# Kernel optimization log

Measured on AMD Instinct MI355X. Metric: run time of the kernel, lower is better.

The kernel has to match this reference:

```python
import jax, jax.numpy as jnp
import numpy as np

B_SZ, D, U, NBR, MH, RH = 16384, 256, 32, 8, 512, 256  # batch, latent, u_dim, branches, meas hidden, rnn hidden
NY = 8 * 2 + 4  # num_prod*2 + num_inj
LN_EPS = 1e-5


def setup_inputs() -> dict:
    key = jax.random.key(0)
    ks = jax.random.split(key, 16)
    inp = {
        "zt": jax.random.normal(ks[0], (B_SZ, D), jnp.float32),
        "dt": jax.random.uniform(ks[1], (1, 1), jnp.float32, 0.1, 1.0),
        "ut": jax.random.normal(ks[2], (B_SZ, U), jnp.float32),
        # stacked per-branch parameters
        "gates": jax.random.normal(ks[3], (NBR, D), jnp.float32) * 0.1,
        "W1": jax.random.normal(ks[4], (NBR, MH, D), jnp.float32) / np.sqrt(D),
        "b1": jnp.zeros((NBR, MH), jnp.float32),
        "ln_g": jnp.ones((NBR, MH), jnp.float32),
        "ln_b": jnp.zeros((NBR, MH), jnp.float32),
        "W2": jax.random.normal(ks[5], (NBR, RH, MH), jnp.float32) / np.sqrt(MH),
        "b2": jnp.zeros((NBR, RH), jnp.float32),
        "lam_r": jnp.zeros((NBR, RH), jnp.float32),
        "lam_i": jax.random.normal(ks[6], (NBR, RH), jnp.float32) * 0.1,
        "rnn_B": jax.random.normal(ks[7], (NBR, RH, RH + U), jnp.float32) / np.sqrt(RH + U),
        "W_out": jax.random.normal(ks[8], (NBR, D, RH), jnp.float32) / np.sqrt(RH),
        "C": jax.random.normal(ks[9], (NY, D), jnp.float32) / np.sqrt(D),
        "Dm": jax.random.normal(ks[10], (NY, U), jnp.float32) / np.sqrt(U),
    }
    return inp


def reference(zt, dt, ut, gates, W1, b1, ln_g, ln_b, W2, b2, lam_r, lam_i, rnn_B, W_out, C, Dm):
    ut_dt = ut * dt                                           # [B, U]
    # spectral gating, all branches at once: [NBR, B, D]
    zg = zt[None, :, :] * jax.nn.sigmoid(gates)[:, None, :]
    # measurement MLP: Linear -> LayerNorm -> GELU (exact) -> Linear
    x = jnp.einsum('nbd,nhd->nbh', zg, W1) + b1[:, None, :]   # [NBR, B, MH]
    mu = jnp.mean(x, axis=-1, keepdims=True)
    var = jnp.mean((x - mu) ** 2, axis=-1, keepdims=True)
    x = (x - mu) / jnp.sqrt(var + LN_EPS) * ln_g[:, None, :] + ln_b[:, None, :]
    x = jax.nn.gelu(x, approximate=False)
    g = jnp.einsum('nbh,nrh->nbr', x, W2) + b2[:, None, :]    # [NBR, B, RH]
    # concat control and apply input matrix B_n
    ut_b = jnp.broadcast_to(ut_dt[None], (gates.shape[0],) + ut_dt.shape)
    inp = jnp.concatenate([g, ut_b], axis=-1)                 # [NBR, B, RH+U]
    b_inp = jnp.einsum('nbi,nri->nbr', inp, rnn_B)            # [NBR, B, RH]
    # single diagonal complex RNN step from h0 = 0:
    #   h_real = 0*lam.r - 0*lam.i + b_inp = b_inp ; h_imag = 0  (lambda drops out)
    h_real = b_inp
    zt1 = jnp.einsum('nbr,ndr->bd', h_real, W_out)            # sum over branches
    yt1 = zt1 @ C.T + ut_dt @ Dm.T
    return zt1, yt1
```

## Files before the change

kernel.cpp:

```cpp
#include <hip/hip_runtime.h>
#include <math.h>

#define B_TOT 16384
#define DD    256
#define UU    32
#define NBR   8
#define MH    512
#define RH    256
#define KIN   288
#define NY    20

typedef unsigned short u16;
typedef __attribute__((ext_vector_type(8))) short bfx8;
typedef __attribute__((ext_vector_type(4))) short bfx4;
typedef __attribute__((ext_vector_type(4))) float fx4;

#define MFMA(a, b, c) __builtin_amdgcn_mfma_f32_16x16x32_bf16((a), (b), (c), 0, 0, 0)

__device__ __forceinline__ u16 f2bf(float f) {
  __bf16 h = (__bf16)f;
  return __builtin_bit_cast(u16, h);
}
__device__ __forceinline__ float fsigmoid(float x) {
  return __builtin_amdgcn_rcpf(1.f + __expf(-x));
}
__device__ __forceinline__ float fgelu(float v) {
  float t = v * v;
  float z = v * __builtin_fmaf(t, 0.07135481627f, 1.5957691216f);
  float p = __expf(z);
  return v - v * __builtin_amdgcn_rcpf(p + 1.f);
}
__device__ __forceinline__ void gload16(const void* g, void* l) {
  __builtin_amdgcn_global_load_lds((const __attribute__((address_space(1))) unsigned int*)(g),
                                   (__attribute__((address_space(3))) unsigned int*)(l),
                                   16, 0, 0);
}

__global__ __launch_bounds__(256)
void skolr_prep(const float* __restrict__ W1, const float* __restrict__ W2,
                const float* __restrict__ rnnB, const float* __restrict__ Wout,
                const float* __restrict__ gates, const float* __restrict__ zt,
                u16* __restrict__ w1g, u16* __restrict__ w2b, u16* __restrict__ bb,
                u16* __restrict__ wotb, u16* __restrict__ ztb)
{
  long i = (long)(blockIdx.x * 256 + threadIdx.x) * 8;
  const long E0 = 1048576;
  const long E1 = 2097152;
  const long E2 = 2686976;
  const long E3 = 3211264;
  const long E4 = 7405568;
  if (i >= E4) return;
  if (i < E0) {
    int n = (int)(i >> 17), h = (int)((i >> 8) & 511), d = (int)(i & 255);
    const float* gp = gates + n * DD + d;
    float4 g0 = *(const float4*)gp, g1 = *(const float4*)(gp + 4);
    float4 a = *(const float4*)(W1 + i), b = *(const float4*)(W1 + i + 4);
    bfx8 v;
    v[0] = f2bf(a.x * fsigmoid(g0.x)); v[1] = f2bf(a.y * fsigmoid(g0.y));
    v[2] = f2bf(a.z * fsigmoid(g0.z)); v[3] = f2bf(a.w * fsigmoid(g0.w));
    v[4] = f2bf(b.x * fsigmoid(g1.x)); v[5] = f2bf(b.y * fsigmoid(g1.y));
    v[6] = f2bf(b.z * fsigmoid(g1.z)); v[7] = f2bf(b.w * fsigmoid(g1.w));
    u16* dst = w1g + (size_t)n * 131072
             + ((((h >> 4) << 3) + (d >> 5)) << 9) + ((h & 15) << 3) + (((d >> 3) & 3) << 7);
    *(bfx8*)dst = v;
    return;
  }
  const float* src; u16* dst; long off;
  if (i < E1) {
    off = i - E0;
    int n = (int)(off >> 17), r = (int)((off >> 9) & 255), k = (int)(off & 511);
    src = W2 + off;
    dst = w2b + (size_t)n * 131072
        + ((((r >> 4) << 4) + (k >> 5)) << 9) + ((r & 15) << 3) + (((k >> 3) & 3) << 7);
  } else if (i < E2) {
    off = i - E1;
    int o = (int)off;
    int n = o / 73728, rem = o - n * 73728;
    int r = rem / KIN, k = rem - r * KIN;
    src = rnnB + off;
    dst = bb + (size_t)n * 73728
        + (((r >> 4) * 9 + (k >> 5)) << 9) + ((r & 15) << 3) + (((k >> 3) & 3) << 7);
  } else if (i < E3) {
    off = i - E2;
    int n = (int)(off >> 16), rem = (int)(off & 65535);
    int d = rem >> 8, r = rem & 255;
    src = Wout + off;
    dst = wotb + ((((d >> 4) << 6) + (n << 3) + (r >> 5)) << 9)
        + ((d & 15) << 3) + (((r >> 3) & 3) << 7);
  } else {
    off = i - E3;
    src = zt + off;
    dst = ztb + off;
  }
  float4 a = *(const float4*)src, b = *(const float4*)(src + 4);
  bfx8 v;
  v[0] = f2bf(a.x); v[1] = f2bf(a.y); v[2] = f2bf(a.z); v[3] = f2bf(a.w);
  v[4] = f2bf(b.x); v[5] = f2bf(b.y); v[6] = f2bf(b.z); v[7] = f2bf(b.w);
  *(bfx8*)dst = v;
}

__global__ __launch_bounds__(512, 2)
void skolr_fused(const u16* __restrict__ ztb, const float* __restrict__ dtp,
                 const float* __restrict__ ut,
                 const u16* __restrict__ w1g, const float* __restrict__ b1,
                 const float* __restrict__ lng, const float* __restrict__ lnb,
                 const u16* __restrict__ w2g, const float* __restrict__ b2v,
                 const u16* __restrict__ rnnb, u16* __restrict__ bing)
{
  __shared__ __align__(16) char smX[65536];
  __shared__ __align__(16) float smR[1024];
  const int tid = threadIdx.x;
  const int w  = tid >> 6;
  const int l  = tid & 63;
  const int lr = l & 15;
  const int lg = l >> 4;
  const int n  = blockIdx.x;
  const int b0 = blockIdx.y * 64;

  #pragma unroll
  for (int j = 0; j < 4; ++j) {
    int q = (w << 2) + j;
    int r = (q << 1) + (l >> 5);
    const u16* src = ztb + (size_t)(b0 + r) * DD + (((l & 31) ^ (r & 7)) << 3);
    gload16(src, smX + (q << 10));
  }
  __syncthreads();

  fx4 acc1[4][4];
  #pragma unroll
  for (int mt = 0; mt < 4; ++mt)
    #pragma unroll
    for (int nt = 0; nt < 4; ++nt)
      acc1[mt][nt] = (fx4){0.f, 0.f, 0.f, 0.f};
  {
    const u16* w1pk = w1g + (size_t)n * 131072;
    #pragma unroll
    for (int kk = 0; kk < 8; ++kk) {
      bfx8 bfr[4];
      #pragma unroll
      for (int nt = 0; nt < 4; ++nt) {
        int b = nt * 16 + lr;
        bfr[nt] = *(const bfx8*)(smX + b * 512 + ((((kk << 2) + lg) ^ (b & 7)) << 4));
      }
      #pragma unroll
      for (int mt = 0; mt < 4; ++mt) {
        int mtile = (mt < 2 ? (w << 1) + mt : 16 + (w << 1) + (mt - 2));
        bfx8 af = *(const bfx8*)(w1pk + (((mtile << 3) + kk) << 9) + (l << 3));
        #pragma unroll
        for (int nt = 0; nt < 4; ++nt)
          acc1[mt][nt] = MFMA(af, bfr[nt], acc1[mt][nt]);
      }
    }
  }
  #pragma unroll
  for (int mt = 0; mt < 4; ++mt) {
    int hb = (mt < 2 ? (w << 5) + mt * 16 : 256 + (w << 5) + (mt - 2) * 16) + (lg << 2);
    fx4 bv = *(const fx4*)(b1 + n * MH + hb);
    #pragma unroll
    for (int nt = 0; nt < 4; ++nt)
      acc1[mt][nt] += bv;
  }

  #pragma unroll
  for (int nt = 0; nt < 4; ++nt) {
    float s1 = 0.f, s2 = 0.f;
    #pragma unroll
    for (int mt = 0; mt < 4; ++mt)
      #pragma unroll
      for (int r = 0; r < 4; ++r) { float v = acc1[mt][nt][r]; s1 += v; s2 += v * v; }
    s1 += __shfl_xor(s1, 16); s1 += __shfl_xor(s1, 32);
    s2 += __shfl_xor(s2, 16); s2 += __shfl_xor(s2, 32);
    if (l < 16) { smR[w * 64 + nt * 16 + l] = s1; smR[512 + w * 64 + nt * 16 + l] = s2; }
  }
  __syncthreads();

  float meanv[4], rstdv[4];
  #pragma unroll
  for (int nt = 0; nt < 4; ++nt) {
    float ms = 0.f, ss = 0.f;
    #pragma unroll
    for (int wv = 0; wv < 8; ++wv) {
      ms += smR[wv * 64 + nt * 16 + lr];
      ss += smR[512 + wv * 64 + nt * 16 + lr];
    }
    float mean = ms * (1.f / 512.f);
    meanv[nt] = mean;
    rstdv[nt] = rsqrtf(ss * (1.f / 512.f) - mean * mean + 1e-5f);
  }
  #pragma unroll
  for (int mt = 0; mt < 4; ++mt) {
    int htile = (mt < 2 ? (w << 5) + mt * 16 : 256 + (w << 5) + (mt - 2) * 16);
    int hb = htile + (lg << 2);
    fx4 g4 = *(const fx4*)(lng + n * MH + hb);
    fx4 e4 = *(const fx4*)(lnb + n * MH + hb);
    #pragma unroll
    for (int nt = 0; nt < 4; ++nt) {
      #pragma unroll
      for (int r = 0; r < 4; ++r) {
        float v = (acc1[mt][nt][r] - meanv[nt]) * rstdv[nt] * g4[r] + e4[r];
        acc1[mt][nt][r] = fgelu(v);
      }
      int b = nt * 16 + lr;
      bfx4 p;
      p[0] = f2bf(acc1[mt][nt][0]); p[1] = f2bf(acc1[mt][nt][1]);
      p[2] = f2bf(acc1[mt][nt][2]); p[3] = f2bf(acc1[mt][nt][3]);
      int chunk6 = (htile >> 3) + (lg >> 1);
      *(bfx4*)(smX + b * 1024 + ((chunk6 ^ (b & 7)) << 4) + ((lg & 1) << 3)) = p;
    }
  }
  __syncthreads();

  const int r0 = w << 5;
  fx4 acc2[2][4];
  #pragma unroll
  for (int mt = 0; mt < 2; ++mt)
    #pragma unroll
    for (int nt = 0; nt < 4; ++nt)
      acc2[mt][nt] = (fx4){0.f, 0.f, 0.f, 0.f};
  {
    const u16* w2pk = w2g + (size_t)n * 131072;
    #pragma unroll
    for (int kk = 0; kk < 16; ++kk) {
      bfx8 xb[4];
      #pragma unroll
      for (int nt = 0; nt < 4; ++nt) {
        int b = nt * 16 + lr;
        xb[nt] = *(const bfx8*)(smX + b * 1024 + ((((kk << 2) + lg) ^ (b & 7)) << 4));
      }
      #pragma unroll
      for (int mt = 0; mt < 2; ++mt) {
        bfx8 af = *(const bfx8*)(w2pk + (((((w << 1) + mt) << 4) + kk) << 9) + (l << 3));
        #pragma unroll
        for (int nt = 0; nt < 4; ++nt)
          acc2[mt][nt] = MFMA(af, xb[nt], acc2[mt][nt]);
      }
    }
  }
  #pragma unroll
  for (int mt = 0; mt < 2; ++mt) {
    fx4 bz = *(const fx4*)(b2v + n * RH + r0 + mt * 16 + (lg << 2));
    #pragma unroll
    for (int nt = 0; nt < 4; ++nt)
      acc2[mt][nt] += bz;
  }
  __syncthreads();

  #pragma unroll
  for (int mt = 0; mt < 2; ++mt)
    #pragma unroll
    for (int nt = 0; nt < 4; ++nt) {
      int b = nt * 16 + lr;
      bfx4 p;
      p[0] = f2bf(acc2[mt][nt][0]); p[1] = f2bf(acc2[mt][nt][1]);
      p[2] = f2bf(acc2[mt][nt][2]); p[3] = f2bf(acc2[mt][nt][3]);
      int chunk5 = ((r0 + mt * 16) >> 3) + (lg >> 1);
      *(bfx4*)(smX + b * 512 + ((chunk5 ^ (b & 7)) << 4) + ((lg & 1) << 3)) = p;
    }
  __syncthreads();

  const float dtv = dtp[0];
  bfx8 ufrag[4];
  #pragma unroll
  for (int nt = 0; nt < 4; ++nt) {
    const float* up = ut + (size_t)(b0 + nt * 16 + lr) * UU + (lg << 3);
    float4 u0 = *(const float4*)up;
    float4 u1 = *(const float4*)(up + 4);
    bfx8 v;
    v[0] = f2bf(u0.x * dtv); v[1] = f2bf(u0.y * dtv);
    v[2] = f2bf(u0.z * dtv); v[3] = f2bf(u0.w * dtv);
    v[4] = f2bf(u1.x * dtv); v[5] = f2bf(u1.y * dtv);
    v[6] = f2bf(u1.z * dtv); v[7] = f2bf(u1.w * dtv);
    ufrag[nt] = v;
  }

  fx4 acc3[2][4];
  #pragma unroll
  for (int mt = 0; mt < 2; ++mt)
    #pragma unroll
    for (int nt = 0; nt < 4; ++nt)
      acc3[mt][nt] = (fx4){0.f, 0.f, 0.f, 0.f};
  {
    const u16* rpk = rnnb + (size_t)n * 73728;
    #pragma unroll
    for (int kk = 0; kk < 8; ++kk) {
      bfx8 gb[4];
      #pragma unroll
      for (int nt = 0; nt < 4; ++nt) {
        int b = nt * 16 + lr;
        gb[nt] = *(const bfx8*)(smX + b * 512 + ((((kk << 2) + lg) ^ (b & 7)) << 4));
      }
      #pragma unroll
      for (int mt = 0; mt < 2; ++mt) {
        bfx8 af = *(const bfx8*)(rpk + (((((w << 1) + mt) * 9) + kk) << 9) + (l << 3));
        #pragma unroll
        for (int nt = 0; nt < 4; ++nt)
          acc3[mt][nt] = MFMA(af, gb[nt], acc3[mt][nt]);
      }
    }
    #pragma unroll
    for (int mt = 0; mt < 2; ++mt) {
      bfx8 af = *(const bfx8*)(rpk + (((((w << 1) + mt) * 9) + 8) << 9) + (l << 3));
      #pragma unroll
      for (int nt = 0; nt < 4; ++nt)
        acc3[mt][nt] = MFMA(af, ufrag[nt], acc3[mt][nt]);
    }
  }
  #pragma unroll
  for (int mt = 0; mt < 2; ++mt)
    #pragma unroll
    for (int nt = 0; nt < 4; ++nt) {
      int b = nt * 16 + lr;
      bfx4 p;
      p[0] = f2bf(acc3[mt][nt][0]); p[1] = f2bf(acc3[mt][nt][1]);
      p[2] = f2bf(acc3[mt][nt][2]); p[3] = f2bf(acc3[mt][nt][3]);
      int chunk5 = ((r0 + mt * 16) >> 3) + (lg >> 1);
      *(bfx4*)(smX + 32768 + b * 512 + ((chunk5 ^ (b & 7)) << 4) + ((lg & 1) << 3)) = p;
    }
  __syncthreads();

  {
    int c = tid & 31;
    #pragma unroll
    for (int j = 0; j < 4; ++j) {
      int row = (tid >> 5) + j * 16;
      int4 v = *(const int4*)(smX + 32768 + row * 512 + (c << 4));
      *(int4*)(bing + (size_t)(b0 + row) * 2048 + n * 256 + c * 8) = v;
    }
  }
}

__global__ __launch_bounds__(512, 2)
void skolr_final(const u16* __restrict__ bing, const u16* __restrict__ wotb,
                 const float* __restrict__ ut, const float* __restrict__ dtp,
                 const float* __restrict__ Cm, const float* __restrict__ Dm,
                 float* __restrict__ outp)
{
  __shared__ __align__(16) char sB[65536];
  const int tid = threadIdx.x;
  const int w  = tid >> 6;
  const int l  = tid & 63;
  const int lr = l & 15;
  const int lg = l >> 4;
  const int b0 = blockIdx.x * 64;

  fx4 acc[2][4];
  #pragma unroll
  for (int mt = 0; mt < 2; ++mt)
    #pragma unroll
    for (int nt = 0; nt < 4; ++nt)
      acc[mt][nt] = (fx4){0.f, 0.f, 0.f, 0.f};

  const int srow = tid >> 5;
  const int scol = tid & 31;
  #define STAGE(buf, ks)                                                        \
    {                                                                           \
      _Pragma("unroll")                                                         \
      for (int j = 0; j < 4; ++j) {                                             \
        const u16* src = bing + (size_t)(b0 + j * 16 + srow) * 2048             \
                              + ((ks) << 8) + (scol << 3);                      \
        void* ldst = sB + (buf) * 32768 + (j << 13) + (w << 10);                \
        gload16(src, ldst);                                                     \
      }                                                                         \
    }

  STAGE(0, 0)
  for (int ks = 0; ks < 8; ++ks) {
    if (ks < 7) {
      STAGE((ks + 1) & 1, ks + 1)
      asm volatile("s_waitcnt vmcnt(4)" ::: "memory");
    } else {
      asm volatile("s_waitcnt vmcnt(0)" ::: "memory");
    }
    __builtin_amdgcn_s_barrier();
    const char* cur = sB + (ks & 1) * 32768;
    #pragma unroll
    for (int kk = 0; kk < 8; ++kk) {
      bfx8 bf[4];
      #pragma unroll
      for (int nt = 0; nt < 4; ++nt) {
        int b = nt * 16 + lr;
        bf[nt] = *(const bfx8*)(cur + b * 512 + ((((kk << 2) + lg) ^ (b & 7)) << 4));
      }
      #pragma unroll
      for (int mt = 0; mt < 2; ++mt) {
        bfx8 af = *(const bfx8*)(wotb + (((((w << 1) + mt) << 6) + (ks << 3) + kk) << 9) + (l << 3));
        #pragma unroll
        for (int nt = 0; nt < 4; ++nt)
          acc[mt][nt] = MFMA(af, bf[nt], acc[mt][nt]);
      }
    }
    __builtin_amdgcn_s_barrier();
  }

  #pragma unroll
  for (int mt = 0; mt < 2; ++mt)
    #pragma unroll
    for (int nt = 0; nt < 4; ++nt) {
      int bl = nt * 16 + lr;
      int d  = (w << 5) + mt * 16 + (lg << 2);
      *(fx4*)(outp + (size_t)(b0 + bl) * DD + d) = acc[mt][nt];
      bfx4 p;
      p[0] = f2bf(acc[mt][nt][0]); p[1] = f2bf(acc[mt][nt][1]);
      p[2] = f2bf(acc[mt][nt][2]); p[3] = f2bf(acc[mt][nt][3]);
      int chunk5 = d >> 3;
      *(bfx4*)(sB + bl * 512 + ((chunk5 ^ (bl & 7)) << 4) + ((lg & 1) << 3)) = p;
    }
  __syncthreads();

  const float dtv = dtp[0];
  for (int i = tid; i < 64 * NY; i += 512) {
    int b = i / NY;
    int y = i - b * NY;
    float s = 0.f;
    #pragma unroll 4
    for (int dc = 0; dc < 32; ++dc) {
      bfx8 zv = *(const bfx8*)(sB + b * 512 + ((dc ^ (b & 7)) << 4));
      const float* cp = Cm + y * DD + dc * 8;
      float4 c0 = *(const float4*)cp;
      float4 c1 = *(const float4*)(cp + 4);
      float z0 = (float)__builtin_bit_cast(__bf16, (u16)zv[0]);
      float z1 = (float)__builtin_bit_cast(__bf16, (u16)zv[1]);
      float z2 = (float)__builtin_bit_cast(__bf16, (u16)zv[2]);
      float z3 = (float)__builtin_bit_cast(__bf16, (u16)zv[3]);
      float z4 = (float)__builtin_bit_cast(__bf16, (u16)zv[4]);
      float z5 = (float)__builtin_bit_cast(__bf16, (u16)zv[5]);
      float z6 = (float)__builtin_bit_cast(__bf16, (u16)zv[6]);
      float z7 = (float)__builtin_bit_cast(__bf16, (u16)zv[7]);
      s += z0 * c0.x + z1 * c0.y + z2 * c0.z + z3 * c0.w;
      s += z4 * c1.x + z5 * c1.y + z6 * c1.z + z7 * c1.w;
    }
    const float* up = ut + (size_t)(b0 + b) * UU;
    const float* dp = Dm + y * UU;
    float s2 = 0.f;
    #pragma unroll
    for (int u = 0; u < UU; u += 4) {
      float4 uu = *(const float4*)(up + u);
      float4 dd = *(const float4*)(dp + u);
      s2 += uu.x * dd.x + uu.y * dd.y + uu.z * dd.z + uu.w * dd.w;
    }
    outp[(size_t)B_TOT * DD + (size_t)(b0 + b) * NY + y] = s + dtv * s2;
  }
}

extern "C" void kernel_launch(void* const* d_in, const int* in_sizes, int n_in,
                              void* d_out, int out_size, void* d_ws, size_t ws_size,
                              hipStream_t stream)
{
  (void)in_sizes; (void)n_in; (void)out_size; (void)ws_size;
  const float* zt    = (const float*)d_in[0];
  const float* dtp   = (const float*)d_in[1];
  const float* ut    = (const float*)d_in[2];
  const float* gates = (const float*)d_in[3];
  const float* W1    = (const float*)d_in[4];
  const float* b1    = (const float*)d_in[5];
  const float* lng   = (const float*)d_in[6];
  const float* lnb   = (const float*)d_in[7];
  const float* W2    = (const float*)d_in[8];
  const float* b2    = (const float*)d_in[9];
  const float* rnnB  = (const float*)d_in[12];
  const float* Wout  = (const float*)d_in[13];
  const float* Cm    = (const float*)d_in[14];
  const float* Dm    = (const float*)d_in[15];
  float* outp = (float*)d_out;
  char* ws = (char*)d_ws;

  u16* w1g  = (u16*)(ws + 0);
  u16* w2b  = (u16*)(ws + 2097152);
  u16* bb   = (u16*)(ws + 4194304);
  u16* wotb = (u16*)(ws + 5373952);
  u16* ztb  = (u16*)(ws + 6422528);
  u16* bing = (u16*)(ws + 14811136);

  skolr_prep<<<3616, 256, 0, stream>>>(W1, W2, rnnB, Wout, gates, zt,
                                       w1g, w2b, bb, wotb, ztb);
  skolr_fused<<<dim3(8, 256), 512, 0, stream>>>(ztb, dtp, ut, w1g, b1, lng, lnb,
                                                w2b, b2, bb, bing);
  skolr_final<<<256, 512, 0, stream>>>(bing, wotb, ut, dtp, Cm, Dm, outp);
}
```

Before: 316.7 us.

## Shrink fused kernel tile to 32 rows with 256 threads and split LDS staging

The fused MLP/RNN kernel now processes 32 batch rows per block with 4 waves instead of 64 rows with 8 waves. Shared memory drops from 64KB to 32KB by splitting the GELU activations into two halves: the first half is staged into one buffer, the second half into another, and the second GEMM runs in two K-phases. This is meant to raise occupancy and the number of blocks per CU. The cost is that each weight fragment is reused across fewer batch columns, so global weight traffic per output rises, and there are more barriers.

```diff
diff --git a/kernel.cpp b/kernel.cpp
--- a/kernel.cpp
+++ b/kernel.cpp
@@ -99,7 +99,7 @@
   *(bfx8*)dst = v;
 }
 
-__global__ __launch_bounds__(512, 2)
+__global__ __launch_bounds__(256, 4)
 void skolr_fused(const u16* __restrict__ ztb, const float* __restrict__ dtp,
                  const float* __restrict__ ut,
                  const u16* __restrict__ w1g, const float* __restrict__ b1,
@@ -107,161 +107,181 @@
                  const u16* __restrict__ w2g, const float* __restrict__ b2v,
                  const u16* __restrict__ rnnb, u16* __restrict__ bing)
 {
-  __shared__ __align__(16) char smX[65536];
-  __shared__ __align__(16) float smR[1024];
+  __shared__ __align__(16) char smX[32768];
+  __shared__ __align__(16) float smR[256];
   const int tid = threadIdx.x;
   const int w  = tid >> 6;
   const int l  = tid & 63;
   const int lr = l & 15;
   const int lg = l >> 4;
   const int n  = blockIdx.x;
-  const int b0 = blockIdx.y * 64;
+  const int b0 = blockIdx.y * 32;
+  char* P = smX;
+  char* Q = smX + 16384;
 
   #pragma unroll
   for (int j = 0; j < 4; ++j) {
-    int q = (w << 2) + j;
+    int q = (j << 2) + w;
     int r = (q << 1) + (l >> 5);
     const u16* src = ztb + (size_t)(b0 + r) * DD + (((l & 31) ^ (r & 7)) << 3);
-    gload16(src, smX + (q << 10));
-  }
-  __syncthreads();
-
-  fx4 acc1[4][4];
-  #pragma unroll
-  for (int mt = 0; mt < 4; ++mt)
-    #pragma unroll
-    for (int nt = 0; nt < 4; ++nt)
+    gload16(src, P + (q << 10));
+  }
+  __syncthreads();
+
+  fx4 acc1[8][2];
+  #pragma unroll
+  for (int mt = 0; mt < 8; ++mt)
+    #pragma unroll
+    for (int nt = 0; nt < 2; ++nt)
       acc1[mt][nt] = (fx4){0.f, 0.f, 0.f, 0.f};
   {
     const u16* w1pk = w1g + (size_t)n * 131072;
     #pragma unroll
     for (int kk = 0; kk < 8; ++kk) {
-      bfx8 bfr[4];
-      #pragma unroll
-      for (int nt = 0; nt < 4; ++nt) {
+      bfx8 bfr[2];
+      #pragma unroll
+      for (int nt = 0; nt < 2; ++nt) {
         int b = nt * 16 + lr;
-        bfr[nt] = *(const bfx8*)(smX + b * 512 + ((((kk << 2) + lg) ^ (b & 7)) << 4));
-      }
-      #pragma unroll
-      for (int mt = 0; mt < 4; ++mt) {
-        int mtile = (mt < 2 ? (w << 1) + mt : 16 + (w << 1) + (mt - 2));
+        bfr[nt] = *(const bfx8*)(P + b * 512 + ((((kk << 2) + lg) ^ (b & 7)) << 4));
+      }
+      #pragma unroll
+      for (int mt = 0; mt < 8; ++mt) {
+        int mtile = (mt < 4 ? (w << 2) + mt : 16 + (w << 2) + (mt - 4));
         bfx8 af = *(const bfx8*)(w1pk + (((mtile << 3) + kk) << 9) + (l << 3));
         #pragma unroll
-        for (int nt = 0; nt < 4; ++nt)
+        for (int nt = 0; nt < 2; ++nt)
           acc1[mt][nt] = MFMA(af, bfr[nt], acc1[mt][nt]);
       }
     }
   }
   #pragma unroll
-  for (int mt = 0; mt < 4; ++mt) {
-    int hb = (mt < 2 ? (w << 5) + mt * 16 : 256 + (w << 5) + (mt - 2) * 16) + (lg << 2);
+  for (int mt = 0; mt < 8; ++mt) {
+    int hb = (mt < 4 ? (w << 6) + mt * 16 : 256 + (w << 6) + (mt - 4) * 16) + (lg << 2);
     fx4 bv = *(const fx4*)(b1 + n * MH + hb);
     #pragma unroll
-    for (int nt = 0; nt < 4; ++nt)
+    for (int nt = 0; nt < 2; ++nt)
       acc1[mt][nt] += bv;
   }
 
   #pragma unroll
-  for (int nt = 0; nt < 4; ++nt) {
+  for (int nt = 0; nt < 2; ++nt) {
     float s1 = 0.f, s2 = 0.f;
     #pragma unroll
-    for (int mt = 0; mt < 4; ++mt)
+    for (int mt = 0; mt < 8; ++mt)
       #pragma unroll
       for (int r = 0; r < 4; ++r) { float v = acc1[mt][nt][r]; s1 += v; s2 += v * v; }
     s1 += __shfl_xor(s1, 16); s1 += __shfl_xor(s1, 32);
     s2 += __shfl_xor(s2, 16); s2 += __shfl_xor(s2, 32);
-    if (l < 16) { smR[w * 64 + nt * 16 + l] = s1; smR[512 + w * 64 + nt * 16 + l] = s2; }
-  }
-  __syncthreads();
-
-  float meanv[4], rstdv[4];
-  #pragma unroll
-  for (int nt = 0; nt < 4; ++nt) {
+    if (l < 16) { smR[(w << 5) + nt * 16 + l] = s1; smR[128 + (w << 5) + nt * 16 + l] = s2; }
+  }
+  __syncthreads();
+
+  float meanv[2], rstdv[2];
+  #pragma unroll
+  for (int nt = 0; nt < 2; ++nt) {
     float ms = 0.f, ss = 0.f;
     #pragma unroll
-    for (int wv = 0; wv < 8; ++wv) {
-      ms += smR[wv * 64 + nt * 16 + lr];
-      ss += smR[512 + wv * 64 + nt * 16 + lr];
+    for (int wv = 0; wv < 4; ++wv) {
+      ms += smR[(wv << 5) + nt * 16 + lr];
+      ss += smR[128 + (wv << 5) + nt * 16 + lr];
     }
     float mean = ms * (1.f / 512.f);
     meanv[nt] = mean;
     rstdv[nt] = rsqrtf(ss * (1.f / 512.f) - mean * mean + 1e-5f);
   }
   #pragma unroll
-  for (int mt = 0; mt < 4; ++mt) {
-    int htile = (mt < 2 ? (w << 5) + mt * 16 : 256 + (w << 5) + (mt - 2) * 16);
-    int hb = htile + (lg << 2);
+  for (int mt = 0; mt < 8; ++mt) {
+    int hb = (mt < 4 ? (w << 6) + mt * 16 : 256 + (w << 6) + (mt - 4) * 16) + (lg << 2);
     fx4 g4 = *(const fx4*)(lng + n * MH + hb);
     fx4 e4 = *(const fx4*)(lnb + n * MH + hb);
     #pragma unroll
-    for (int nt = 0; nt < 4; ++nt) {
+    for (int nt = 0; nt < 2; ++nt)
       #pragma unroll
       for (int r = 0; r < 4; ++r) {
         float v = (acc1[mt][nt][r] - meanv[nt]) * rstdv[nt] * g4[r] + e4[r];
         acc1[mt][nt][r] = fgelu(v);
       }
+  }
+
+  #pragma unroll
+  for (int mt = 0; mt < 4; ++mt)
+    #pragma unroll
+    for (int nt = 0; nt < 2; ++nt) {
       int b = nt * 16 + lr;
       bfx4 p;
       p[0] = f2bf(acc1[mt][nt][0]); p[1] = f2bf(acc1[mt][nt][1]);
       p[2] = f2bf(acc1[mt][nt][2]); p[3] = f2bf(acc1[mt][nt][3]);
-      int chunk6 = (htile >> 3) + (lg >> 1);
-      *(bfx4*)(smX + b * 1024 + ((chunk6 ^ (b & 7)) << 4) + ((lg & 1) << 3)) = p;
-    }
-  }
-  __syncthreads();
-
-  const int r0 = w << 5;
-  fx4 acc2[2][4];
-  #pragma unroll
-  for (int mt = 0; mt < 2; ++mt)
-    #pragma unroll
-    for (int nt = 0; nt < 4; ++nt)
+      int ch = (w << 3) + (mt << 1) + (lg >> 1);
+      *(bfx4*)(Q + b * 512 + ((ch ^ (b & 7)) << 4) + ((lg & 1) << 3)) = p;
+    }
+  __syncthreads();
+
+  fx4 acc2[4][2];
+  #pragma unroll
+  for (int mt = 0; mt < 4; ++mt)
+    #pragma unroll
+    for (int nt = 0; nt < 2; ++nt)
       acc2[mt][nt] = (fx4){0.f, 0.f, 0.f, 0.f};
-  {
-    const u16* w2pk = w2g + (size_t)n * 131072;
-    #pragma unroll
-    for (int kk = 0; kk < 16; ++kk) {
-      bfx8 xb[4];
-      #pragma unroll
-      for (int nt = 0; nt < 4; ++nt) {
-        int b = nt * 16 + lr;
-        xb[nt] = *(const bfx8*)(smX + b * 1024 + ((((kk << 2) + lg) ^ (b & 7)) << 4));
-      }
-      #pragma unroll
-      for (int mt = 0; mt < 2; ++mt) {
-        bfx8 af = *(const bfx8*)(w2pk + (((((w << 1) + mt) << 4) + kk) << 9) + (l << 3));
-        #pragma unroll
-        for (int nt = 0; nt < 4; ++nt)
-          acc2[mt][nt] = MFMA(af, xb[nt], acc2[mt][nt]);
-      }
-    }
-  }
-  #pragma unroll
-  for (int mt = 0; mt < 2; ++mt) {
-    fx4 bz = *(const fx4*)(b2v + n * RH + r0 + mt * 16 + (lg << 2));
-    #pragma unroll
-    for (int nt = 0; nt < 4; ++nt)
-      acc2[mt][nt] += bz;
-  }
-  __syncthreads();
-
-  #pragma unroll
-  for (int mt = 0; mt < 2; ++mt)
-    #pragma unroll
-    for (int nt = 0; nt < 4; ++nt) {
+  const u16* w2pk = w2g + (size_t)n * 131072;
+  #pragma unroll
+  for (int kk = 0; kk < 8; ++kk) {
+    bfx8 xb[2];
+    #pragma unroll
+    for (int nt = 0; nt < 2; ++nt) {
+      int b = nt * 16 + lr;
+      xb[nt] = *(const bfx8*)(Q + b * 512 + ((((kk << 2) + lg) ^ (b & 7)) << 4));
+    }
+    #pragma unroll
+    for (int mt = 0; mt < 4; ++mt) {
+      bfx8 af = *(const bfx8*)(w2pk + (((((w << 2) + mt) << 4) + kk) << 9) + (l << 3));
+      #pragma unroll
+      for (int nt = 0; nt < 2; ++nt)
+        acc2[mt][nt] = MFMA(af, xb[nt], acc2[mt][nt]);
+    }
+  }
+  __syncthreads();
+
+  #pragma unroll
+  for (int mt = 4; mt < 8; ++mt)
+    #pragma unroll
+    for (int nt = 0; nt < 2; ++nt) {
       int b = nt * 16 + lr;
       bfx4 p;
-      p[0] = f2bf(acc2[mt][nt][0]); p[1] = f2bf(acc2[mt][nt][1]);
-      p[2] = f2bf(acc2[mt][nt][2]); p[3] = f2bf(acc2[mt][nt][3]);
-      int chunk5 = ((r0 + mt * 16) >> 3) + (lg >> 1);
-      *(bfx4*)(smX + b * 512 + ((chunk5 ^ (b & 7)) << 4) + ((lg & 1) << 3)) = p;
-    }
-  __syncthreads();
+      p[0] = f2bf(acc1[mt][nt][0]); p[1] = f2bf(acc1[mt][nt][1]);
+      p[2] = f2bf(acc1[mt][nt][2]); p[3] = f2bf(acc1[mt][nt][3]);
+      int ch = (w << 3) + ((mt - 4) << 1) + (lg >> 1);
+      *(bfx4*)(P + b * 512 + ((ch ^ (b & 7)) << 4) + ((lg & 1) << 3)) = p;
+    }
+  __syncthreads();
+
+  #pragma unroll
+  for (int kk = 8; kk < 16; ++kk) {
+    bfx8 xb[2];
+    #pragma unroll
+    for (int nt = 0; nt < 2; ++nt) {
+      int b = nt * 16 + lr;
+      xb[nt] = *(const bfx8*)(P + b * 512 + (((((kk - 8) << 2) + lg) ^ (b & 7)) << 4));
+    }
+    #pragma unroll
+    for (int mt = 0; mt < 4; ++mt) {
+      bfx8 af = *(const bfx8*)(w2pk + (((((w << 2) + mt) << 4) + kk) << 9) + (l << 3));
+      #pragma unroll
+      for (int nt = 0; nt < 2; ++nt)
+        acc2[mt][nt] = MFMA(af, xb[nt], acc2[mt][nt]);
+    }
+  }
+  #pragma unroll
+  for (int mt = 0; mt < 4; ++mt) {
+    fx4 bz = *(const fx4*)(b2v + n * RH + (w << 6) + mt * 16 + (lg << 2));
+    #pragma unroll
+    for (int nt = 0; nt < 2; ++nt)
+      acc2[mt][nt] += bz;
+  }
 
   const float dtv = dtp[0];
-  bfx8 ufrag[4];
-  #pragma unroll
-  for (int nt = 0; nt < 4; ++nt) {
+  bfx8 ufrag[2];
+  #pragma unroll
+  for (int nt = 0; nt < 2; ++nt) {
     const float* up = ut + (size_t)(b0 + nt * 16 + lr) * UU + (lg << 3);
     float4 u0 = *(const float4*)up;
     float4 u1 = *(const float4*)(up + 4);
@@ -273,59 +293,71 @@
     ufrag[nt] = v;
   }
 
-  fx4 acc3[2][4];
-  #pragma unroll
-  for (int mt = 0; mt < 2; ++mt)
-    #pragma unroll
-    for (int nt = 0; nt < 4; ++nt)
+  #pragma unroll
+  for (int mt = 0; mt < 4; ++mt)
+    #pragma unroll
+    for (int nt = 0; nt < 2; ++nt) {
+      int b = nt * 16 + lr;
+      bfx4 p;
+      p[0] = f2bf(acc2[mt][nt][0]); p[1] = f2bf(acc2[mt][nt][1]);
+      p[2] = f2bf(acc2[mt][nt][2]); p[3] = f2bf(acc2[mt][nt][3]);
+      int ch = (w << 3) + (mt << 1) + (lg >> 1);
+      *(bfx4*)(Q + b * 512 + ((ch ^ (b & 7)) << 4) + ((lg & 1) << 3)) = p;
+    }
+  __syncthreads();
+
+  fx4 acc3[4][2];
+  #pragma unroll
+  for (int mt = 0; mt < 4; ++mt)
+    #pragma unroll
+    for (int nt = 0; nt < 2; ++nt)
       acc3[mt][nt] = (fx4){0.f, 0.f, 0.f, 0.f};
   {
     const u16* rpk = rnnb + (size_t)n * 73728;
     #pragma unroll
     for (int kk = 0; kk < 8; ++kk) {
-      bfx8 gb[4];
-      #pragma unroll
-      for (int nt = 0; nt < 4; ++nt) {
+      bfx8 gb[2];
+      #pragma unroll
+      for (int nt = 0; nt < 2; ++nt) {
         int b = nt * 16 + lr;
-        gb[nt] = *(const bfx8*)(smX + b * 512 + ((((kk << 2) + lg) ^ (b & 7)) << 4));
-      }
-      #pragma unroll
-      for (int mt = 0; mt < 2; ++mt) {
-        bfx8 af = *(const bfx8*)(rpk + (((((w << 1) + mt) * 9) + kk) << 9) + (l << 3));
+        gb[nt] = *(const bfx8*)(Q + b * 512 + ((((kk << 2) + lg) ^ (b & 7)) << 4));
+      }
+      #pragma unroll
+      for (int mt = 0; mt < 4; ++mt) {
+        bfx8 af = *(const bfx8*)(rpk + (((((w << 2) + mt) * 9) + kk) << 9) + (l << 3));
         #pragma unroll
-        for (int nt = 0; nt < 4; ++nt)
+        for (int nt = 0; nt < 2; ++nt)
           acc3[mt][nt] = MFMA(af, gb[nt], acc3[mt][nt]);
       }
     }
     #pragma unroll
-    for (int mt = 0; mt < 2; ++mt) {
-      bfx8 af = *(const bfx8*)(rpk + (((((w << 1) + mt) * 9) + 8) << 9) + (l << 3));
-      #pragma unroll
-      for (int nt = 0; nt < 4; ++nt)
+    for (int mt = 0; mt < 4; ++mt) {
+      bfx8 af = *(const bfx8*)(rpk + (((((w << 2) + mt) * 9) + 8) << 9) + (l << 3));
+      #pragma unroll
+      for (int nt = 0; nt < 2; ++nt)
         acc3[mt][nt] = MFMA(af, ufrag[nt], acc3[mt][nt]);
     }
   }
-  #pragma unroll
-  for (int mt = 0; mt < 2; ++mt)
-    #pragma unroll
-    for (int nt = 0; nt < 4; ++nt) {
+
+  #pragma unroll
+  for (int mt = 0; mt < 4; ++mt)
+    #pragma unroll
+    for (int nt = 0; nt < 2; ++nt) {
       int b = nt * 16 + lr;
       bfx4 p;
       p[0] = f2bf(acc3[mt][nt][0]); p[1] = f2bf(acc3[mt][nt][1]);
       p[2] = f2bf(acc3[mt][nt][2]); p[3] = f2bf(acc3[mt][nt][3]);
-      int chunk5 = ((r0 + mt * 16) >> 3) + (lg >> 1);
-      *(bfx4*)(smX + 32768 + b * 512 + ((chunk5 ^ (b & 7)) << 4) + ((lg & 1) << 3)) = p;
-    }
-  __syncthreads();
-
-  {
+      int ch = (w << 3) + (mt << 1) + (lg >> 1);
+      *(bfx4*)(P + b * 512 + ((ch ^ (b & 7)) << 4) + ((lg & 1) << 3)) = p;
+    }
+  __syncthreads();
+
+  #pragma unroll
+  for (int j = 0; j < 4; ++j) {
+    int row = (tid >> 5) + (j << 3);
     int c = tid & 31;
-    #pragma unroll
-    for (int j = 0; j < 4; ++j) {
-      int row = (tid >> 5) + j * 16;
-      int4 v = *(const int4*)(smX + 32768 + row * 512 + (c << 4));
-      *(int4*)(bing + (size_t)(b0 + row) * 2048 + n * 256 + c * 8) = v;
-    }
+    int4 v = *(const int4*)(P + row * 512 + (c << 4));
+    *(int4*)(bing + (size_t)(b0 + row) * 2048 + n * 256 + c * 8) = v;
   }
 }
 
@@ -473,7 +505,7 @@
 
   skolr_prep<<<3616, 256, 0, stream>>>(W1, W2, rnnB, Wout, gates, zt,
                                        w1g, w2b, bb, wotb, ztb);
-  skolr_fused<<<dim3(8, 256), 512, 0, stream>>>(ztb, dtp, ut, w1g, b1, lng, lnb,
+  skolr_fused<<<dim3(8, 512), 256, 0, stream>>>(ztb, dtp, ut, w1g, b1, lng, lnb,
                                                 w2b, b2, bb, bing);
   skolr_final<<<256, 512, 0, stream>>>(bing, wotb, ut, dtp, Cm, Dm, outp);
 }
```

Result: slower. 388.5 us (+22.7%).

## Fuse per-branch W_out GEMM into main kernel and reduce partials separately

Applied to the files above, without the earlier changes.

Moves the W_out projection into the fused per-branch kernel, so each block multiplies its own branch's RNN output by that branch's W_out slice and writes a bf16 partial zt1 per branch. A new lightweight kernel sums the eight branch partials in fp32, writes zt1, and computes yt1 from an fp32 shared-memory copy. This removes the separate 2048-wide K-loop GEMM kernel and its double-buffered staging. In exchange, the fused kernel does more work and bf16 rounding now happens per branch before summation.

```diff
diff --git a/kernel.cpp b/kernel.cpp
--- a/kernel.cpp
+++ b/kernel.cpp
@@ -20,6 +20,10 @@
 __device__ __forceinline__ u16 f2bf(float f) {
   __bf16 h = (__bf16)f;
   return __builtin_bit_cast(u16, h);
+}
+__device__ __forceinline__ float bf2f(u16 u) {
+  union { unsigned u; float f; } v; v.u = ((unsigned)u) << 16;
+  return v.f;
 }
 __device__ __forceinline__ float fsigmoid(float x) {
   return __builtin_amdgcn_rcpf(1.f + __expf(-x));
@@ -85,8 +89,8 @@
     int n = (int)(off >> 16), rem = (int)(off & 65535);
     int d = rem >> 8, r = rem & 255;
     src = Wout + off;
-    dst = wotb + ((((d >> 4) << 6) + (n << 3) + (r >> 5)) << 9)
-        + ((d & 15) << 3) + (((r >> 3) & 3) << 7);
+    dst = wotb + (size_t)n * 65536
+        + ((((d >> 4) << 3) + (r >> 5)) << 9) + ((d & 15) << 3) + (((r >> 3) & 3) << 7);
   } else {
     off = i - E3;
     src = zt + off;
@@ -105,7 +109,8 @@
                  const u16* __restrict__ w1g, const float* __restrict__ b1,
                  const float* __restrict__ lng, const float* __restrict__ lnb,
                  const u16* __restrict__ w2g, const float* __restrict__ b2v,
-                 const u16* __restrict__ rnnb, u16* __restrict__ bing)
+                 const u16* __restrict__ rnnb, const u16* __restrict__ wotpk,
+                 u16* __restrict__ zt1p)
 {
   __shared__ __align__(16) char smX[65536];
   __shared__ __align__(16) float smR[1024];
@@ -318,116 +323,99 @@
     }
   __syncthreads();
 
+  fx4 acc4[2][4];
+  #pragma unroll
+  for (int mt = 0; mt < 2; ++mt)
+    #pragma unroll
+    for (int nt = 0; nt < 4; ++nt)
+      acc4[mt][nt] = (fx4){0.f, 0.f, 0.f, 0.f};
+  {
+    const u16* opk = wotpk + (size_t)n * 65536;
+    #pragma unroll
+    for (int kk = 0; kk < 8; ++kk) {
+      bfx8 bf[4];
+      #pragma unroll
+      for (int nt = 0; nt < 4; ++nt) {
+        int b = nt * 16 + lr;
+        bf[nt] = *(const bfx8*)(smX + 32768 + b * 512 + ((((kk << 2) + lg) ^ (b & 7)) << 4));
+      }
+      #pragma unroll
+      for (int mt = 0; mt < 2; ++mt) {
+        bfx8 af = *(const bfx8*)(opk + (((((w << 1) + mt) << 3) + kk) << 9) + (l << 3));
+        #pragma unroll
+        for (int nt = 0; nt < 4; ++nt)
+          acc4[mt][nt] = MFMA(af, bf[nt], acc4[mt][nt]);
+      }
+    }
+  }
+  #pragma unroll
+  for (int mt = 0; mt < 2; ++mt)
+    #pragma unroll
+    for (int nt = 0; nt < 4; ++nt) {
+      int b = nt * 16 + lr;
+      bfx4 p;
+      p[0] = f2bf(acc4[mt][nt][0]); p[1] = f2bf(acc4[mt][nt][1]);
+      p[2] = f2bf(acc4[mt][nt][2]); p[3] = f2bf(acc4[mt][nt][3]);
+      int chunk5 = ((r0 + mt * 16) >> 3) + (lg >> 1);
+      *(bfx4*)(smX + b * 512 + ((chunk5 ^ (b & 7)) << 4) + ((lg & 1) << 3)) = p;
+    }
+  __syncthreads();
+
   {
     int c = tid & 31;
     #pragma unroll
     for (int j = 0; j < 4; ++j) {
       int row = (tid >> 5) + j * 16;
-      int4 v = *(const int4*)(smX + 32768 + row * 512 + (c << 4));
-      *(int4*)(bing + (size_t)(b0 + row) * 2048 + n * 256 + c * 8) = v;
-    }
-  }
-}
-
-__global__ __launch_bounds__(512, 2)
-void skolr_final(const u16* __restrict__ bing, const u16* __restrict__ wotb,
-                 const float* __restrict__ ut, const float* __restrict__ dtp,
-                 const float* __restrict__ Cm, const float* __restrict__ Dm,
-                 float* __restrict__ outp)
+      int4 v = *(const int4*)(smX + row * 512 + (c << 4));
+      *(int4*)(zt1p + (size_t)n * 4194304 + (size_t)(b0 + row) * 256 + c * 8) = v;
+    }
+  }
+}
+
+__global__ __launch_bounds__(256)
+void skolr_reduce_y(const u16* __restrict__ zt1p, const float* __restrict__ ut,
+                    const float* __restrict__ dtp, const float* __restrict__ Cm,
+                    const float* __restrict__ Dm, float* __restrict__ outp)
 {
-  __shared__ __align__(16) char sB[65536];
+  __shared__ float sZ[64][260];
   const int tid = threadIdx.x;
-  const int w  = tid >> 6;
-  const int l  = tid & 63;
-  const int lr = l & 15;
-  const int lg = l >> 4;
   const int b0 = blockIdx.x * 64;
 
-  fx4 acc[2][4];
-  #pragma unroll
-  for (int mt = 0; mt < 2; ++mt)
-    #pragma unroll
-    for (int nt = 0; nt < 4; ++nt)
-      acc[mt][nt] = (fx4){0.f, 0.f, 0.f, 0.f};
-
-  const int srow = tid >> 5;
-  const int scol = tid & 31;
-  #define STAGE(buf, ks)                                                        \
-    {                                                                           \
-      _Pragma("unroll")                                                         \
-      for (int j = 0; j < 4; ++j) {                                             \
-        const u16* src = bing + (size_t)(b0 + j * 16 + srow) * 2048             \
-                              + ((ks) << 8) + (scol << 3);                      \
-        void* ldst = sB + (buf) * 32768 + (j << 13) + (w << 10);                \
-        gload16(src, ldst);                                                     \
-      }                                                                         \
-    }
-
-  STAGE(0, 0)
-  for (int ks = 0; ks < 8; ++ks) {
-    if (ks < 7) {
-      STAGE((ks + 1) & 1, ks + 1)
-      asm volatile("s_waitcnt vmcnt(4)" ::: "memory");
-    } else {
-      asm volatile("s_waitcnt vmcnt(0)" ::: "memory");
-    }
-    __builtin_amdgcn_s_barrier();
-    const char* cur = sB + (ks & 1) * 32768;
-    #pragma unroll
-    for (int kk = 0; kk < 8; ++kk) {
-      bfx8 bf[4];
-      #pragma unroll
-      for (int nt = 0; nt < 4; ++nt) {
-        int b = nt * 16 + lr;
-        bf[nt] = *(const bfx8*)(cur + b * 512 + ((((kk << 2) + lg) ^ (b & 7)) << 4));
-      }
-      #pragma unroll
-      for (int mt = 0; mt < 2; ++mt) {
-        bfx8 af = *(const bfx8*)(wotb + (((((w << 1) + mt) << 6) + (ks << 3) + kk) << 9) + (l << 3));
-        #pragma unroll
-        for (int nt = 0; nt < 4; ++nt)
-          acc[mt][nt] = MFMA(af, bf[nt], acc[mt][nt]);
-      }
-    }
-    __builtin_amdgcn_s_barrier();
-  }
-
-  #pragma unroll
-  for (int mt = 0; mt < 2; ++mt)
-    #pragma unroll
-    for (int nt = 0; nt < 4; ++nt) {
-      int bl = nt * 16 + lr;
-      int d  = (w << 5) + mt * 16 + (lg << 2);
-      *(fx4*)(outp + (size_t)(b0 + bl) * DD + d) = acc[mt][nt];
-      bfx4 p;
-      p[0] = f2bf(acc[mt][nt][0]); p[1] = f2bf(acc[mt][nt][1]);
-      p[2] = f2bf(acc[mt][nt][2]); p[3] = f2bf(acc[mt][nt][3]);
-      int chunk5 = d >> 3;
-      *(bfx4*)(sB + bl * 512 + ((chunk5 ^ (bl & 7)) << 4) + ((lg & 1) << 3)) = p;
-    }
+  #pragma unroll
+  for (int p = 0; p < 8; ++p) {
+    int q = tid + (p << 8);
+    int row = q >> 5, c = q & 31;
+    size_t off = (size_t)(b0 + row) * 256 + c * 8;
+    float s0 = 0.f, s1 = 0.f, s2 = 0.f, s3 = 0.f, s4 = 0.f, s5 = 0.f, s6 = 0.f, s7 = 0.f;
+    #pragma unroll
+    for (int n = 0; n < 8; ++n) {
+      bfx8 v = *(const bfx8*)(zt1p + (size_t)n * 4194304 + off);
+      s0 += bf2f((u16)v[0]); s1 += bf2f((u16)v[1]);
+      s2 += bf2f((u16)v[2]); s3 += bf2f((u16)v[3]);
+      s4 += bf2f((u16)v[4]); s5 += bf2f((u16)v[5]);
+      s6 += bf2f((u16)v[6]); s7 += bf2f((u16)v[7]);
+    }
+    int d0 = (c ^ (row & 7)) << 3;
+    float* op = outp + (size_t)(b0 + row) * DD + d0;
+    *(float4*)op       = (float4){s0, s1, s2, s3};
+    *(float4*)(op + 4) = (float4){s4, s5, s6, s7};
+    float* zp = &sZ[row][d0];
+    *(float4*)zp       = (float4){s0, s1, s2, s3};
+    *(float4*)(zp + 4) = (float4){s4, s5, s6, s7};
+  }
   __syncthreads();
 
   const float dtv = dtp[0];
-  for (int i = tid; i < 64 * NY; i += 512) {
+  for (int i = tid; i < 64 * NY; i += 256) {
     int b = i / NY;
     int y = i - b * NY;
+    const float* cp = Cm + y * DD;
     float s = 0.f;
-    #pragma unroll 4
-    for (int dc = 0; dc < 32; ++dc) {
-      bfx8 zv = *(const bfx8*)(sB + b * 512 + ((dc ^ (b & 7)) << 4));
-      const float* cp = Cm + y * DD + dc * 8;
-      float4 c0 = *(const float4*)cp;
-      float4 c1 = *(const float4*)(cp + 4);
-      float z0 = (float)__builtin_bit_cast(__bf16, (u16)zv[0]);
-      float z1 = (float)__builtin_bit_cast(__bf16, (u16)zv[1]);
-      float z2 = (float)__builtin_bit_cast(__bf16, (u16)zv[2]);
-      float z3 = (float)__builtin_bit_cast(__bf16, (u16)zv[3]);
-      float z4 = (float)__builtin_bit_cast(__bf16, (u16)zv[4]);
-      float z5 = (float)__builtin_bit_cast(__bf16, (u16)zv[5]);
-      float z6 = (float)__builtin_bit_cast(__bf16, (u16)zv[6]);
-      float z7 = (float)__builtin_bit_cast(__bf16, (u16)zv[7]);
-      s += z0 * c0.x + z1 * c0.y + z2 * c0.z + z3 * c0.w;
-      s += z4 * c1.x + z5 * c1.y + z6 * c1.z + z7 * c1.w;
+    #pragma unroll 8
+    for (int dc = 0; dc < 64; ++dc) {
+      float4 z = *(const float4*)&sZ[b][dc * 4];
+      float4 c = *(const float4*)(cp + dc * 4);
+      s += z.x * c.x + z.y * c.y + z.z * c.z + z.w * c.w;
     }
     const float* up = ut + (size_t)(b0 + b) * UU;
     const float* dp = Dm + y * UU;
@@ -469,11 +457,11 @@
   u16* bb   = (u16*)(ws + 4194304);
   u16* wotb = (u16*)(ws + 5373952);
   u16* ztb  = (u16*)(ws + 6422528);
-  u16* bing = (u16*)(ws + 14811136);
+  u16* zt1p = (u16*)(ws + 14811136);
 
   skolr_prep<<<3616, 256, 0, stream>>>(W1, W2, rnnB, Wout, gates, zt,
                                        w1g, w2b, bb, wotb, ztb);
   skolr_fused<<<dim3(8, 256), 512, 0, stream>>>(ztb, dtp, ut, w1g, b1, lng, lnb,
-                                                w2b, b2, bb, bing);
-  skolr_final<<<256, 512, 0, stream>>>(bing, wotb, ut, dtp, Cm, Dm, outp);
-}
+                                                w2b, b2, bb, wotb, zt1p);
+  skolr_reduce_y<<<256, 256, 0, stream>>>(zt1p, ut, dtp, Cm, Dm, outp);
+}
```

Result: faster. 307.6 us (-2.9%).
